# Kernel optimization log

Hardware: AMD Instinct MI355X
Metric: run time of the kernel (lower is better)

## Reference

```python
import jax, jax.numpy as jnp
import numpy as np

D_MODEL = 2048
NUM_HEADS = 16
HEAD_DIM = D_MODEL // NUM_HEADS
SEQ = 2048
BATCH = 2
ROPE_BASE = 10000.0
EPS = 1e-5


def _rope_cache(seq_len, head_dim, base):
    inv_freq = 1.0 / (base ** (jnp.arange(0, head_dim, 2, dtype=jnp.float32) / head_dim))
    t = jnp.arange(seq_len, dtype=jnp.float32)
    freqs = jnp.outer(t, inv_freq)                      # [S, hd/2]
    emb = jnp.concatenate([freqs, freqs], axis=-1)      # [S, hd]
    return jnp.cos(emb), jnp.sin(emb)


def _rotate_half(x):
    x1, x2 = jnp.split(x, 2, axis=-1)
    return jnp.concatenate([-x2, x1], axis=-1)


def setup_inputs() -> dict:
    key = jax.random.key(0)
    ks = jax.random.split(key, 8)
    s = 1.0 / np.sqrt(D_MODEL)
    inp = {
        "x": jax.random.normal(ks[0], (SEQ, BATCH, D_MODEL), dtype=jnp.float32),
        "causal_mask": jnp.triu(jnp.ones((SEQ, SEQ), dtype=jnp.bool_), k=1),
        "key_padding_mask": jnp.zeros((BATCH, SEQ), dtype=jnp.bool_),
        "norm_w": jnp.ones((D_MODEL,), dtype=jnp.float32),
        "q_w": jax.random.normal(ks[1], (D_MODEL, D_MODEL), dtype=jnp.float32) * s,
        "q_b": jnp.zeros((D_MODEL,), dtype=jnp.float32),
        "k_w": jax.random.normal(ks[2], (D_MODEL, D_MODEL), dtype=jnp.float32) * s,
        "k_b": jnp.zeros((D_MODEL,), dtype=jnp.float32),
        "v_w": jax.random.normal(ks[3], (D_MODEL, D_MODEL), dtype=jnp.float32) * s,
        "v_b": jnp.zeros((D_MODEL,), dtype=jnp.float32),
        "o_w": jax.random.normal(ks[4], (D_MODEL, D_MODEL), dtype=jnp.float32) * s,
        "o_b": jnp.zeros((D_MODEL,), dtype=jnp.float32),
    }
    return inp


def reference(x, causal_mask, key_padding_mask, norm_w, q_w, q_b, k_w, k_b, v_w, v_b, o_w, o_b):
    seq_len, batch, _ = x.shape
    # RMSNorm variant: x / (||x||_2 + eps) * w  (note: L2 norm, not RMS)
    nrm = jnp.linalg.norm(x, axis=-1, keepdims=True)
    xn = x / (nrm + EPS) * norm_w

    q = (xn @ q_w.T + q_b).reshape(seq_len, batch, NUM_HEADS, HEAD_DIM)
    k = (xn @ k_w.T + k_b).reshape(seq_len, batch, NUM_HEADS, HEAD_DIM)
    v = (xn @ v_w.T + v_b).reshape(seq_len, batch, NUM_HEADS, HEAD_DIM)

    cos, sin = _rope_cache(seq_len, HEAD_DIM, ROPE_BASE)
    cos = cos[:, None, None, :]
    sin = sin[:, None, None, :]
    q = q * cos + _rotate_half(q) * sin
    k = k * cos + _rotate_half(k) * sin

    # [S,B,H,D] -> [B,H,S,D]
    q = q.transpose(1, 2, 0, 3)
    k = k.transpose(1, 2, 0, 3)
    v = v.transpose(1, 2, 0, 3)

    scores = jnp.einsum('bhqd,bhkd->bhqk', q, k) / jnp.sqrt(jnp.float32(HEAD_DIM))
    neg_inf = jnp.float32(-jnp.inf)
    scores = jnp.where(causal_mask[None, None, :, :], neg_inf, scores)
    scores = jnp.where(key_padding_mask[:, None, None, :], neg_inf, scores)

    attn = jax.nn.softmax(scores, axis=-1)
    out = jnp.einsum('bhqk,bhkd->bhqd', attn, v)
    out = out.transpose(2, 0, 1, 3).reshape(seq_len, batch, D_MODEL)  # [S,B,D]
    return out @ o_w.T + o_b
```

## Files before the change

### kernel.cpp

```cpp
#include <hip/hip_runtime.h>
#include <hip/hip_bf16.h>
#include <cstdint>

typedef __attribute__((ext_vector_type(8))) short short8_t;
typedef __attribute__((ext_vector_type(4))) short s16x4;
typedef __attribute__((ext_vector_type(4))) float f32x4;

#define SEQ 2048
#define BATCH 2
#define DM 2048
#define NH 16
#define HD 128
#define SCALE 0.08838834764831845f

__device__ __forceinline__ short f2bf(float f) {
    union { __hip_bfloat16 h; short s; } u; u.h = __float2bfloat16(f); return u.s;
}
__device__ __forceinline__ float bf2f(short s) {
    union { short s; __hip_bfloat16 h; } u; u.s = s; return __bfloat162float(u.h);
}

__global__ void __launch_bounds__(256) prep_kernel(const float* __restrict__ qw,
                                                   const float* __restrict__ kw,
                                                   const float* __restrict__ vw,
                                                   const float* __restrict__ ow,
                                                   short* __restrict__ wqkv,
                                                   const float* __restrict__ x,
                                                   const float* __restrict__ nw,
                                                   short* __restrict__ xn,
                                                   float* __restrict__ cosT,
                                                   float* __restrict__ sinT) {
    const int bid = blockIdx.x;
    const int t = threadIdx.x;
    if (bid < 2048) {
        const int per = DM * DM / 4;
        int i = bid * 256 + t;
        const int stride = 2048 * 256;
        for (; i < 4 * per; i += stride) {
            int region = i / per;
            int off = i - region * per;
            const float* src = region == 0 ? qw : (region == 1 ? kw : (region == 2 ? vw : ow));
            float4 v = ((const float4*)src)[off];
            s16x4 o;
            o[0] = f2bf(v.x); o[1] = f2bf(v.y); o[2] = f2bf(v.z); o[3] = f2bf(v.w);
            ((s16x4*)(wqkv + (size_t)region * DM * DM))[off] = o;
        }
    } else if (bid < 2560) {
        int j = (bid - 2048) * 256 + t;
        int tpos = j >> 6, i = j & 63;
        float inv = exp2f(-(2.0f * (float)i / 128.0f) * log2f(10000.0f));
        float a = (float)tpos * inv;
        cosT[tpos * 64 + i] = cosf(a);
        sinT[tpos * 64 + i] = sinf(a);
    } else {
        __shared__ float red[4];
        int row = bid - 2560;
        const float* xr = x + (size_t)row * DM;
        short* outr = xn + (size_t)row * DM;
        float vals[8];
        float ss = 0.f;
#pragma unroll
        for (int i = 0; i < 8; ++i) { float v = xr[t + 256 * i]; vals[i] = v; ss += v * v; }
#pragma unroll
        for (int off = 1; off < 64; off <<= 1) ss += __shfl_xor(ss, off);
        int lane = t & 63, wv = t >> 6;
        if (lane == 0) red[wv] = ss;
        __syncthreads();
        float tot = red[0] + red[1] + red[2] + red[3];
        float inv = 1.f / (sqrtf(tot) + 1e-5f);
#pragma unroll
        for (int i = 0; i < 8; ++i)
            outr[t + 256 * i] = f2bf(vals[i] * inv * nw[t + 256 * i]);
    }
}

#define DSREAD(d, a) asm volatile("ds_read_b128 %0, %1" : "=v"(d) : "v"(a))

template <int MODE>
__global__ void __launch_bounds__(256) gemm_db(const short* __restrict__ A,
                                               const short* __restrict__ B,
                                               int N, int K,
                                               short* __restrict__ oq, short* __restrict__ ok,
                                               short* __restrict__ ov,
                                               const float* __restrict__ bq,
                                               const float* __restrict__ bk,
                                               const float* __restrict__ bv,
                                               float* __restrict__ outF,
                                               const float* __restrict__ bias) {
    extern __shared__ short lds[];
    const int tid = threadIdx.x;
    const int lane = tid & 63;
    const int w = tid >> 6;
    const int wr = w >> 1, wc = w & 1;
    const int brow = blockIdx.y * 128;
    const int bcol = blockIdx.x * 128;

    const short* gA[4]; const short* gB[4]; int ldsC[4];
#pragma unroll
    for (int p = 0; p < 4; ++p) {
        int c = p * 256 + tid;
        int row = c >> 3;
        int slot = (c & 7) ^ (row & 7);
        gA[p] = A + (size_t)(brow + row) * K + slot * 8;
        gB[p] = B + (size_t)(bcol + row) * K + slot * 8;
        ldsC[p] = c * 8;
    }
    const uint32_t ldsBase = (uint32_t)(uintptr_t)&lds[0];

    f32x4 acc[4][4];
#pragma unroll
    for (int i = 0; i < 4; ++i)
#pragma unroll
        for (int j = 0; j < 4; ++j) acc[i][j] = (f32x4){0.f, 0.f, 0.f, 0.f};

    const int fr = lane & 15;
    const int fs = lane >> 4;
    uint32_t aOff[4][2], bOff[4][2];
#pragma unroll
    for (int i = 0; i < 4; ++i)
#pragma unroll
        for (int ks = 0; ks < 2; ++ks) {
            int ch = (ks * 4 + fs) ^ (fr & 7);
            int ar = wr * 64 + i * 16 + fr;
            int br = wc * 64 + i * 16 + fr;
            aOff[i][ks] = ldsBase + (uint32_t)(ar * 128 + ch * 16);
            bOff[i][ks] = ldsBase + 32768u + (uint32_t)(br * 128 + ch * 16);
        }

    const int nt = K >> 6;
#pragma unroll
    for (int p = 0; p < 4; ++p)
        __builtin_amdgcn_global_load_lds((const __attribute__((address_space(1))) void*)gA[p],
                                         (__attribute__((address_space(3))) void*)(lds + ldsC[p]), 16, 0, 0);
#pragma unroll
    for (int p = 0; p < 4; ++p)
        __builtin_amdgcn_global_load_lds((const __attribute__((address_space(1))) void*)gB[p],
                                         (__attribute__((address_space(3))) void*)(lds + 16384 + ldsC[p]), 16, 0, 0);

    for (int t = 0; t < nt; ++t) {
        const int cur = t & 1;
        if (t + 1 < nt) {
            const int nb = (t + 1) & 1;
            const int kb = (t + 1) << 6;
#pragma unroll
            for (int p = 0; p < 4; ++p)
                __builtin_amdgcn_global_load_lds((const __attribute__((address_space(1))) void*)(gA[p] + kb),
                                                 (__attribute__((address_space(3))) void*)(lds + nb * 8192 + ldsC[p]), 16, 0, 0);
#pragma unroll
            for (int p = 0; p < 4; ++p)
                __builtin_amdgcn_global_load_lds((const __attribute__((address_space(1))) void*)(gB[p] + kb),
                                                 (__attribute__((address_space(3))) void*)(lds + 16384 + nb * 8192 + ldsC[p]), 16, 0, 0);
            asm volatile("s_waitcnt vmcnt(8)" ::: "memory");
        } else {
            asm volatile("s_waitcnt vmcnt(0)" ::: "memory");
        }
        __builtin_amdgcn_s_barrier();

        const uint32_t ab = (uint32_t)(cur * 16384);
        short8_t af[4][2], bfv[4][2];
#pragma unroll
        for (int i = 0; i < 4; ++i)
#pragma unroll
            for (int ks = 0; ks < 2; ++ks) DSREAD(af[i][ks], aOff[i][ks] + ab);
#pragma unroll
        for (int j = 0; j < 4; ++j)
#pragma unroll
            for (int ks = 0; ks < 2; ++ks) DSREAD(bfv[j][ks], bOff[j][ks] + ab);
        asm volatile("s_waitcnt lgkmcnt(0)" ::: "memory");
        __builtin_amdgcn_sched_barrier(0);

        __builtin_amdgcn_s_setprio(1);
#pragma unroll
        for (int ks = 0; ks < 2; ++ks)
#pragma unroll
            for (int i = 0; i < 4; ++i)
#pragma unroll
                for (int j = 0; j < 4; ++j)
                    acc[i][j] = __builtin_amdgcn_mfma_f32_16x16x32_bf16(af[i][ks], bfv[j][ks], acc[i][j], 0, 0, 0);
        __builtin_amdgcn_s_setprio(0);
        __builtin_amdgcn_s_barrier();
    }

    const int fq = (lane >> 4) * 4;
#pragma unroll
    for (int i = 0; i < 4; ++i) {
        int mrow = brow + wr * 64 + i * 16 + fq;
#pragma unroll
        for (int j = 0; j < 4; ++j) {
            int ncol = bcol + wc * 64 + j * 16 + fr;
            if (MODE == 0) {
                int which = ncol >> 11;
                int hl = ncol & 2047;
                int h = hl >> 7, d = hl & 127;
                const float* bp = which == 0 ? bq : (which == 1 ? bk : bv);
                short* dst = which == 0 ? oq : (which == 1 ? ok : ov);
                float bval = bp[hl];
#pragma unroll
                for (int jj = 0; jj < 4; ++jj) {
                    int m = mrow + jj;
                    int s = m >> 1, b = m & 1;
                    float v = acc[i][j][jj] + bval;
                    size_t idx;
                    if (which == 2)
                        idx = (((size_t)(b * NH + h)) * HD + d) * SEQ + s;
                    else
                        idx = (((size_t)(b * NH + h)) * SEQ + s) * HD + d;
                    dst[idx] = f2bf(v);
                }
            } else {
                float bval = bias[ncol];
#pragma unroll
                for (int jj = 0; jj < 4; ++jj) {
                    int m = mrow + jj;
                    outF[(size_t)m * N + ncol] = acc[i][j][jj] + bval;
                }
            }
        }
    }
}

__global__ void __launch_bounds__(256) rope_k_kernel(short* __restrict__ k,
                                                     const float* __restrict__ cosT,
                                                     const float* __restrict__ sinT) {
    int w = threadIdx.x >> 6, lane = threadIdx.x & 63;
    int idx = blockIdx.x * 4 + w;
    int s = idx & (SEQ - 1);
    size_t base = (size_t)idx * HD;
    float c = cosT[s * 64 + lane], sn = sinT[s * 64 + lane];
    float k1 = bf2f(k[base + lane]), k2 = bf2f(k[base + lane + 64]);
    k[base + lane] = f2bf(k1 * c - k2 * sn);
    k[base + lane + 64] = f2bf(k2 * c + k1 * sn);
}

__global__ void __launch_bounds__(512) attn_kernel(const short* __restrict__ Q,
                                                   const short* __restrict__ K,
                                                   const short* __restrict__ V,
                                                   const float* __restrict__ cosT,
                                                   const float* __restrict__ sinT,
                                                   short* __restrict__ AO) {
    __shared__ short Kl[64 * 136];
    __shared__ short Vt[128 * 88];
    __shared__ short Pl[8][16 * 88];

    const int bh = blockIdx.x;
    const int qt = blockIdx.y;
    const int b = bh >> 4;
    const int h = bh & 15;
    const size_t base = (size_t)bh * (SEQ * HD);
    const int tid = threadIdx.x;
    const int lane = tid & 63;
    const int w = tid >> 6;
    const int fr = lane & 15;
    const int fk = (lane >> 4) * 8;
    const int fq = (lane >> 4) * 4;
    const int qbase = qt * 128 + w * 16;
    const int qg = qbase + fr;

    const int kr = tid >> 4;
    const int kc8 = (tid & 15) * 8;
    const int vd = tid >> 3;
    const int vc8 = (tid & 7) * 8;

    short8_t qf[4];
#pragma unroll
    for (int kc = 0; kc < 4; ++kc)
        qf[kc] = *(const short8_t*)&Q[base + (size_t)(qg) * HD + kc * 32 + fk];

    {
        const float* cb = cosT + (size_t)qg * 64;
        const float* sb = sinT + (size_t)qg * 64;
#pragma unroll
        for (int kc = 0; kc < 2; ++kc) {
            float4 c0 = *(const float4*)&cb[kc * 32 + fk];
            float4 c1 = *(const float4*)&cb[kc * 32 + fk + 4];
            float4 s0 = *(const float4*)&sb[kc * 32 + fk];
            float4 s1 = *(const float4*)&sb[kc * 32 + fk + 4];
            float cv[8] = {c0.x, c0.y, c0.z, c0.w, c1.x, c1.y, c1.z, c1.w};
            float sv[8] = {s0.x, s0.y, s0.z, s0.w, s1.x, s1.y, s1.z, s1.w};
#pragma unroll
            for (int e = 0; e < 8; ++e) {
                float q1 = bf2f(qf[kc][e]), q2 = bf2f(qf[kc + 2][e]);
                qf[kc][e]     = f2bf((q1 * cv[e] - q2 * sv[e]) * SCALE);
                qf[kc + 2][e] = f2bf((q2 * cv[e] + q1 * sv[e]) * SCALE);
            }
        }
    }

    f32x4 acc[8];
#pragma unroll
    for (int dt = 0; dt < 8; ++dt) acc[dt] = (f32x4){0.f, 0.f, 0.f, 0.f};
    float m_r = -1e30f, l_r = 0.f;

    const int ktmax = qt * 2 + 1;

    short8_t kreg[2], vreg[2];
#pragma unroll
    for (int p = 0; p < 2; ++p) {
        kreg[p] = *(const short8_t*)&K[base + (size_t)(p * 32 + kr) * HD + kc8];
        vreg[p] = *(const short8_t*)&V[base + (size_t)(p * 64 + vd) * SEQ + vc8];
    }
#pragma unroll
    for (int p = 0; p < 2; ++p) {
        *(short8_t*)&Kl[(p * 32 + kr) * 136 + kc8] = kreg[p];
        *(short8_t*)&Vt[(p * 64 + vd) * 88 + vc8] = vreg[p];
    }
    __syncthreads();

    for (int kt = 0; kt <= ktmax; ++kt) {
        const bool active = (kt * 64 <= qbase + 15);
        f32x4 st[4];
        if (active) {
            __builtin_amdgcn_s_setprio(1);
#pragma unroll
            for (int nt = 0; nt < 4; ++nt) {
                f32x4 a = (f32x4){0.f, 0.f, 0.f, 0.f};
#pragma unroll
                for (int kc = 0; kc < 4; ++kc) {
                    short8_t kf = *(const short8_t*)&Kl[(nt * 16 + fr) * 136 + kc * 32 + fk];
                    a = __builtin_amdgcn_mfma_f32_16x16x32_bf16(kf, qf[kc], a, 0, 0, 0);
                }
                st[nt] = a;
            }
            __builtin_amdgcn_s_setprio(0);
        }

        if (kt < ktmax) {
            const size_t kb2 = base + (size_t)((kt + 1) * 64) * HD;
            const size_t vb2 = base + (size_t)(kt + 1) * 64;
#pragma unroll
            for (int p = 0; p < 2; ++p) {
                kreg[p] = *(const short8_t*)&K[kb2 + (size_t)(p * 32 + kr) * HD + kc8];
                vreg[p] = *(const short8_t*)&V[vb2 + (size_t)(p * 64 + vd) * SEQ + vc8];
            }
        }

        if (active) {
            const bool needMask = (kt * 64 + 63 > qbase);
            float rmax = -1e30f;
            if (needMask) {
#pragma unroll
                for (int nt = 0; nt < 4; ++nt)
#pragma unroll
                    for (int jj = 0; jj < 4; ++jj) {
                        int kg = kt * 64 + nt * 16 + fq + jj;
                        float sv = st[nt][jj];
                        sv = (kg > qg) ? -1e30f : sv;
                        st[nt][jj] = sv;
                        rmax = fmaxf(rmax, sv);
                    }
            } else {
#pragma unroll
                for (int nt = 0; nt < 4; ++nt)
#pragma unroll
                    for (int jj = 0; jj < 4; ++jj) rmax = fmaxf(rmax, st[nt][jj]);
            }
            rmax = fmaxf(rmax, __shfl_xor(rmax, 16));
            rmax = fmaxf(rmax, __shfl_xor(rmax, 32));

            const bool doRescale = !(m_r > -1e29f && __all(rmax - m_r <= 8.0f));
            float m_new = doRescale ? fmaxf(m_r, rmax) : m_r;
            float rsum = 0.f;
#pragma unroll
            for (int nt = 0; nt < 4; ++nt) {
                s16x4 pk;
#pragma unroll
                for (int jj = 0; jj < 4; ++jj) {
                    float p = __expf(st[nt][jj] - m_new);
                    rsum += p;
                    pk[jj] = f2bf(p);
                }
                *(s16x4*)&Pl[w][fr * 88 + nt * 16 + fq] = pk;
            }
            rsum += __shfl_xor(rsum, 16);
            rsum += __shfl_xor(rsum, 32);
            if (doRescale) {
                float corr = __expf(m_r - m_new);
                l_r = l_r * corr + rsum;
                m_r = m_new;
                float c4[4];
#pragma unroll
                for (int jj = 0; jj < 4; ++jj) c4[jj] = __shfl(corr, fq + jj);
#pragma unroll
                for (int dt = 0; dt < 8; ++dt)
#pragma unroll
                    for (int jj = 0; jj < 4; ++jj) acc[dt][jj] *= c4[jj];
            } else {
                l_r += rsum;
            }

            __builtin_amdgcn_s_setprio(1);
#pragma unroll
            for (int kc = 0; kc < 2; ++kc) {
                short8_t pf = *(const short8_t*)&Pl[w][fr * 88 + kc * 32 + fk];
#pragma unroll
                for (int dt = 0; dt < 8; ++dt) {
                    short8_t vf = *(const short8_t*)&Vt[(dt * 16 + fr) * 88 + kc * 32 + fk];
                    acc[dt] = __builtin_amdgcn_mfma_f32_16x16x32_bf16(pf, vf, acc[dt], 0, 0, 0);
                }
            }
            __builtin_amdgcn_s_setprio(0);
        }

        __syncthreads();
        if (kt < ktmax) {
#pragma unroll
            for (int p = 0; p < 2; ++p) {
                *(short8_t*)&Kl[(p * 32 + kr) * 136 + kc8] = kreg[p];
                *(short8_t*)&Vt[(p * 64 + vd) * 88 + vc8] = vreg[p];
            }
            __syncthreads();
        }
    }

    float linv[4];
#pragma unroll
    for (int jj = 0; jj < 4; ++jj) linv[jj] = 1.f / __shfl(l_r, fq + jj);
#pragma unroll
    for (int dt = 0; dt < 8; ++dt) {
#pragma unroll
        for (int jj = 0; jj < 4; ++jj) {
            int qrow = qbase + fq + jj;
            int d = dt * 16 + fr;
            AO[((size_t)(qrow * BATCH + b)) * DM + h * HD + d] = f2bf(acc[dt][jj] * linv[jj]);
        }
    }
}

extern "C" void kernel_launch(void* const* d_in, const int* in_sizes, int n_in,
                              void* d_out, int out_size, void* d_ws, size_t ws_size,
                              hipStream_t stream) {
    (void)in_sizes; (void)n_in; (void)out_size; (void)ws_size;
    const float* x  = (const float*)d_in[0];
    const float* nw = (const float*)d_in[3];
    const float* qw = (const float*)d_in[4];
    const float* qbias = (const float*)d_in[5];
    const float* kw = (const float*)d_in[6];
    const float* kbias = (const float*)d_in[7];
    const float* vw = (const float*)d_in[8];
    const float* vbias = (const float*)d_in[9];
    const float* ow = (const float*)d_in[10];
    const float* obias = (const float*)d_in[11];
    float* out = (float*)d_out;

    char* ws = (char*)d_ws;
    size_t off = 0;
    float* cosT = (float*)(ws + off); off += (size_t)SEQ * 64 * 4;
    float* sinT = (float*)(ws + off); off += (size_t)SEQ * 64 * 4;
    short* wqkv = (short*)(ws + off); off += (size_t)3 * DM * DM * 2;
    short* wo   = (short*)(ws + off); off += (size_t)DM * DM * 2;
    short* xn   = (short*)(ws + off); off += (size_t)SEQ * BATCH * DM * 2;
    short* qd   = (short*)(ws + off); off += (size_t)SEQ * BATCH * DM * 2;
    short* kd   = (short*)(ws + off); off += (size_t)SEQ * BATCH * DM * 2;
    short* vd   = (short*)(ws + off); off += (size_t)SEQ * BATCH * DM * 2;
    short* ao   = xn;

    hipFuncSetAttribute((const void*)gemm_db<0>, hipFuncAttributeMaxDynamicSharedMemorySize, 65536);
    hipFuncSetAttribute((const void*)gemm_db<1>, hipFuncAttributeMaxDynamicSharedMemorySize, 65536);

    prep_kernel<<<2560 + SEQ * BATCH, 256, 0, stream>>>(qw, kw, vw, ow, wqkv, x, nw, xn, cosT, sinT);
    gemm_db<0><<<dim3(3 * DM / 128, SEQ * BATCH / 128), 256, 65536, stream>>>(
        xn, wqkv, 3 * DM, DM, qd, kd, vd, qbias, kbias, vbias, nullptr, nullptr);
    rope_k_kernel<<<BATCH * NH * SEQ / 4, 256, 0, stream>>>(kd, cosT, sinT);
    attn_kernel<<<dim3(BATCH * NH, SEQ / 128), 512, 0, stream>>>(qd, kd, vd, cosT, sinT, ao);
    gemm_db<1><<<dim3(DM / 128, SEQ * BATCH / 128), 256, 65536, stream>>>(
        ao, wo, DM, DM, nullptr, nullptr, nullptr, nullptr, nullptr, nullptr, out, obias);
}
```

Measured before the change: 259.7 us.

## Replace QKV projection GEMM with 256x256-tile 8-wave ping-pong kernel

The fused QKV projection moves from the 128x128 double-buffered GEMM to a new 512-thread kernel with 256x256 output tiles and 128KB of LDS. Tiles are staged in half-blocks via direct global-to-LDS loads, interleaved with MFMA quarter-steps, and a blockIdx swizzle groups neighbouring tiles for L2 reuse. The intent is more data reuse per loaded byte and better overlap of loads with MFMA work. The cost is heavy register pressure (a 32-entry accumulator array) and delicate hand-counted waitcnt/barrier sequencing. The DSREAD constraint also becomes early-clobber.

```diff
diff --git a/kernel.cpp b/kernel.cpp
--- a/kernel.cpp
+++ b/kernel.cpp
@@ -19,6 +19,8 @@
 __device__ __forceinline__ float bf2f(short s) {
     union { short s; __hip_bfloat16 h; } u; u.s = s; return __bfloat162float(u.h);
 }
+
+#define DSREAD(d, a) asm volatile("ds_read_b128 %0, %1" : "=&v"(d) : "v"(a))
 
 __global__ void __launch_bounds__(256) prep_kernel(const float* __restrict__ qw,
                                                    const float* __restrict__ kw,
@@ -74,17 +76,224 @@
     }
 }
 
-#define DSREAD(d, a) asm volatile("ds_read_b128 %0, %1" : "=v"(d) : "v"(a))
+__device__ __forceinline__ void stage_half(const short* __restrict__ G, int gRow0, int K, int kOff,
+                                           short* ldsBase, int w, int lane) {
+#pragma unroll
+    for (int j = 0; j < 2; ++j) {
+        int c = j * 512 + w * 64 + lane;
+        int row = c >> 3;
+        int slot = (c & 7) ^ (row & 7);
+        const short* g = G + (size_t)(gRow0 + row) * K + kOff + slot * 8;
+        __builtin_amdgcn_global_load_lds((const __attribute__((address_space(1))) void*)g,
+                                         (__attribute__((address_space(3))) void*)(ldsBase + (j * 512 + w * 64) * 8),
+                                         16, 0, 0);
+    }
+}
+
+__device__ __forceinline__ void q16(f32x4 (&acc)[8][4], short8_t (&aa)[4][2], short8_t (&bb)[4][2],
+                                    int ib, int jb) {
+#pragma unroll
+    for (int ks = 0; ks < 2; ++ks)
+#pragma unroll
+        for (int ii = 0; ii < 4; ++ii)
+#pragma unroll
+            for (int jj = 0; jj < 2; ++jj)
+                acc[ib + ii][jb + jj] = __builtin_amdgcn_mfma_f32_16x16x32_bf16(
+                    aa[ii][ks], bb[jb + jj][ks], acc[ib + ii][jb + jj], 0, 0, 0);
+}
+
+template <bool LAST>
+__device__ __forceinline__ void kpair(short* lds, uint32_t uA, uint32_t uAx, uint32_t uB, uint32_t uBx,
+                                      const short* __restrict__ A, const short* __restrict__ B,
+                                      int brow, int bcol, int K, int it,
+                                      f32x4 (&acc)[8][4], int w, int lane) {
+    const int t1 = 2 * it + 1, p0 = 2 * it + 2, p1 = 2 * it + 3;
+    short* ldsA = lds;
+    short* ldsB = lds + 32768;
+    short8_t af[4][2], bf[4][2], ag[4][2];
+
+#pragma unroll
+    for (int i = 0; i < 4; ++i) { DSREAD(af[i][0], uA + i * 2048); DSREAD(af[i][1], uAx + i * 2048); }
+#pragma unroll
+    for (int j = 0; j < 2; ++j) { DSREAD(bf[j][0], uB + j * 2048); DSREAD(bf[j][1], uBx + j * 2048); }
+    stage_half(A, brow + 128, K, t1 * 64, ldsA + 24576, w, lane);
+    asm volatile("s_waitcnt lgkmcnt(8)" ::: "memory");
+    __builtin_amdgcn_s_barrier();
+    asm volatile("s_waitcnt lgkmcnt(0)" ::: "memory");
+    __builtin_amdgcn_sched_barrier(0);
+    __builtin_amdgcn_s_setprio(1);
+    q16(acc, af, bf, 0, 0);
+    __builtin_amdgcn_s_setprio(0);
+    __builtin_amdgcn_s_barrier();
+
+#pragma unroll
+    for (int j = 2; j < 4; ++j) { DSREAD(bf[j][0], uB + j * 2048); DSREAD(bf[j][1], uBx + j * 2048); }
+    __builtin_amdgcn_s_barrier();
+    asm volatile("s_waitcnt lgkmcnt(0)" ::: "memory");
+    __builtin_amdgcn_sched_barrier(0);
+    __builtin_amdgcn_s_setprio(1);
+    q16(acc, af, bf, 0, 2);
+    __builtin_amdgcn_s_setprio(0);
+    __builtin_amdgcn_s_barrier();
+
+#pragma unroll
+    for (int i = 0; i < 4; ++i) { DSREAD(ag[i][0], uA + (i + 4) * 2048); DSREAD(ag[i][1], uAx + (i + 4) * 2048); }
+    if (!LAST) stage_half(B, bcol, K, p0 * 64, ldsB, w, lane);
+    __builtin_amdgcn_s_barrier();
+    asm volatile("s_waitcnt lgkmcnt(0)" ::: "memory");
+    __builtin_amdgcn_sched_barrier(0);
+    __builtin_amdgcn_s_setprio(1);
+    q16(acc, ag, bf, 4, 0);
+    __builtin_amdgcn_s_setprio(0);
+    __builtin_amdgcn_s_barrier();
+
+    if (!LAST) {
+        stage_half(B, bcol + 128, K, p0 * 64, ldsB + 8192, w, lane);
+        stage_half(A, brow, K, p0 * 64, ldsA, w, lane);
+    }
+    __builtin_amdgcn_s_barrier();
+    __builtin_amdgcn_s_setprio(1);
+    q16(acc, ag, bf, 4, 2);
+    __builtin_amdgcn_s_setprio(0);
+    if (!LAST) asm volatile("s_waitcnt vmcnt(6)" ::: "memory");
+    else       asm volatile("s_waitcnt vmcnt(0)" ::: "memory");
+    __builtin_amdgcn_s_barrier();
+
+#pragma unroll
+    for (int i = 0; i < 4; ++i) { DSREAD(af[i][0], uA + 32768 + i * 2048); DSREAD(af[i][1], uAx + 32768 + i * 2048); }
+#pragma unroll
+    for (int j = 0; j < 2; ++j) { DSREAD(bf[j][0], uB + 32768 + j * 2048); DSREAD(bf[j][1], uBx + 32768 + j * 2048); }
+    if (!LAST) stage_half(A, brow + 128, K, p0 * 64, ldsA + 8192, w, lane);
+    asm volatile("s_waitcnt lgkmcnt(8)" ::: "memory");
+    __builtin_amdgcn_s_barrier();
+    asm volatile("s_waitcnt lgkmcnt(0)" ::: "memory");
+    __builtin_amdgcn_sched_barrier(0);
+    __builtin_amdgcn_s_setprio(1);
+    q16(acc, af, bf, 0, 0);
+    __builtin_amdgcn_s_setprio(0);
+    __builtin_amdgcn_s_barrier();
+
+#pragma unroll
+    for (int j = 2; j < 4; ++j) { DSREAD(bf[j][0], uB + 32768 + j * 2048); DSREAD(bf[j][1], uBx + 32768 + j * 2048); }
+    __builtin_amdgcn_s_barrier();
+    asm volatile("s_waitcnt lgkmcnt(0)" ::: "memory");
+    __builtin_amdgcn_sched_barrier(0);
+    __builtin_amdgcn_s_setprio(1);
+    q16(acc, af, bf, 0, 2);
+    __builtin_amdgcn_s_setprio(0);
+    __builtin_amdgcn_s_barrier();
+
+#pragma unroll
+    for (int i = 0; i < 4; ++i) { DSREAD(ag[i][0], uA + 32768 + (i + 4) * 2048); DSREAD(ag[i][1], uAx + 32768 + (i + 4) * 2048); }
+    if (!LAST) stage_half(B, bcol, K, p1 * 64, ldsB + 16384, w, lane);
+    __builtin_amdgcn_s_barrier();
+    asm volatile("s_waitcnt lgkmcnt(0)" ::: "memory");
+    __builtin_amdgcn_sched_barrier(0);
+    __builtin_amdgcn_s_setprio(1);
+    q16(acc, ag, bf, 4, 0);
+    __builtin_amdgcn_s_setprio(0);
+    __builtin_amdgcn_s_barrier();
+
+    if (!LAST) {
+        stage_half(B, bcol + 128, K, p1 * 64, ldsB + 24576, w, lane);
+        stage_half(A, brow, K, p1 * 64, ldsA + 16384, w, lane);
+    }
+    __builtin_amdgcn_s_barrier();
+    __builtin_amdgcn_s_setprio(1);
+    q16(acc, ag, bf, 4, 2);
+    __builtin_amdgcn_s_setprio(0);
+    if (!LAST) asm volatile("s_waitcnt vmcnt(6)" ::: "memory");
+    __builtin_amdgcn_s_barrier();
+}
+
+__global__ void __launch_bounds__(512, 2) gemm8p(const short* __restrict__ A,
+                                                 const short* __restrict__ B,
+                                                 int Mt, int Nt, int K,
+                                                 short* __restrict__ oq, short* __restrict__ ok,
+                                                 short* __restrict__ ov,
+                                                 const float* __restrict__ bq,
+                                                 const float* __restrict__ bk,
+                                                 const float* __restrict__ bv) {
+    extern __shared__ short lds[];
+    const int tid = threadIdx.x;
+    const int lane = tid & 63;
+    const int w = tid >> 6;
+    const int wr = w >> 2;
+    const int wc = w & 3;
+
+    const int nwg = Mt * Nt;
+    const int cpx = nwg >> 3;
+    const int bid = blockIdx.x;
+    const int swz = (bid & 7) * cpx + (bid >> 3);
+    const int brow = (swz % Mt) * 256;
+    const int bcol = (swz / Mt) * 256;
+
+    f32x4 acc[8][4];
+#pragma unroll
+    for (int i = 0; i < 8; ++i)
+#pragma unroll
+        for (int j = 0; j < 4; ++j) acc[i][j] = (f32x4){0.f, 0.f, 0.f, 0.f};
+
+    short* ldsA = lds;
+    short* ldsB = lds + 32768;
+
+    const int fr = lane & 15;
+    const int fs = lane >> 4;
+    const int c0 = fs ^ (fr & 7);
+    const uint32_t ldsBase = (uint32_t)(uintptr_t)&lds[0];
+    const uint32_t uA  = ldsBase + (uint32_t)(wr * 16384 + fr * 128 + c0 * 16);
+    const uint32_t uAx = ldsBase + (uint32_t)(wr * 16384 + fr * 128 + (c0 ^ 4) * 16);
+    const uint32_t uB  = ldsBase + 65536u + (uint32_t)((wc >> 1) * 16384 + (wc & 1) * 8192 + fr * 128 + c0 * 16);
+    const uint32_t uBx = ldsBase + 65536u + (uint32_t)((wc >> 1) * 16384 + (wc & 1) * 8192 + fr * 128 + (c0 ^ 4) * 16);
+
+    stage_half(B, bcol,       K, 0,  ldsB,          w, lane);
+    stage_half(B, bcol + 128, K, 0,  ldsB + 8192,   w, lane);
+    stage_half(A, brow,       K, 0,  ldsA,          w, lane);
+    stage_half(A, brow + 128, K, 0,  ldsA + 8192,   w, lane);
+    stage_half(B, bcol,       K, 64, ldsB + 16384,  w, lane);
+    stage_half(B, bcol + 128, K, 64, ldsB + 24576,  w, lane);
+    stage_half(A, brow,       K, 64, ldsA + 16384,  w, lane);
+    asm volatile("s_waitcnt vmcnt(6)" ::: "memory");
+    __builtin_amdgcn_s_barrier();
+
+    const int niter = K / 128;
+    for (int it = 0; it < niter - 1; ++it)
+        kpair<false>(lds, uA, uAx, uB, uBx, A, B, brow, bcol, K, it, acc, w, lane);
+    kpair<true>(lds, uA, uAx, uB, uBx, A, B, brow, bcol, K, niter - 1, acc, w, lane);
+
+    const int fq = (lane >> 4) * 4;
+#pragma unroll
+    for (int i = 0; i < 8; ++i) {
+        int mrow = brow + wr * 128 + i * 16 + fq;
+#pragma unroll
+        for (int j = 0; j < 4; ++j) {
+            int ncol = bcol + wc * 64 + j * 16 + fr;
+            int which = ncol >> 11;
+            int hl = ncol & 2047;
+            int h = hl >> 7, d = hl & 127;
+            const float* bp = which == 0 ? bq : (which == 1 ? bk : bv);
+            short* dst = which == 0 ? oq : (which == 1 ? ok : ov);
+            float bval = bp[hl];
+#pragma unroll
+            for (int jj = 0; jj < 4; ++jj) {
+                int m = mrow + jj;
+                int s = m >> 1, b = m & 1;
+                float v = acc[i][j][jj] + bval;
+                size_t idx;
+                if (which == 2)
+                    idx = (((size_t)(b * NH + h)) * HD + d) * SEQ + s;
+                else
+                    idx = (((size_t)(b * NH + h)) * SEQ + s) * HD + d;
+                dst[idx] = f2bf(v);
+            }
+        }
+    }
+}
 
 template <int MODE>
 __global__ void __launch_bounds__(256) gemm_db(const short* __restrict__ A,
                                                const short* __restrict__ B,
                                                int N, int K,
-                                               short* __restrict__ oq, short* __restrict__ ok,
-                                               short* __restrict__ ov,
-                                               const float* __restrict__ bq,
-                                               const float* __restrict__ bk,
-                                               const float* __restrict__ bv,
                                                float* __restrict__ outF,
                                                const float* __restrict__ bias) {
     extern __shared__ short lds[];
@@ -188,32 +397,11 @@
 #pragma unroll
         for (int j = 0; j < 4; ++j) {
             int ncol = bcol + wc * 64 + j * 16 + fr;
-            if (MODE == 0) {
-                int which = ncol >> 11;
-                int hl = ncol & 2047;
-                int h = hl >> 7, d = hl & 127;
-                const float* bp = which == 0 ? bq : (which == 1 ? bk : bv);
-                short* dst = which == 0 ? oq : (which == 1 ? ok : ov);
-                float bval = bp[hl];
-#pragma unroll
-                for (int jj = 0; jj < 4; ++jj) {
-                    int m = mrow + jj;
-                    int s = m >> 1, b = m & 1;
-                    float v = acc[i][j][jj] + bval;
-                    size_t idx;
-                    if (which == 2)
-                        idx = (((size_t)(b * NH + h)) * HD + d) * SEQ + s;
-                    else
-                        idx = (((size_t)(b * NH + h)) * SEQ + s) * HD + d;
-                    dst[idx] = f2bf(v);
-                }
-            } else {
-                float bval = bias[ncol];
-#pragma unroll
-                for (int jj = 0; jj < 4; ++jj) {
-                    int m = mrow + jj;
-                    outF[(size_t)m * N + ncol] = acc[i][j][jj] + bval;
-                }
+            float bval = bias[ncol];
+#pragma unroll
+            for (int jj = 0; jj < 4; ++jj) {
+                int m = mrow + jj;
+                outF[(size_t)m * N + ncol] = acc[i][j][jj] + bval;
             }
         }
     }
@@ -454,14 +642,14 @@
     short* vd   = (short*)(ws + off); off += (size_t)SEQ * BATCH * DM * 2;
     short* ao   = xn;
 
-    hipFuncSetAttribute((const void*)gemm_db<0>, hipFuncAttributeMaxDynamicSharedMemorySize, 65536);
+    hipFuncSetAttribute((const void*)gemm8p, hipFuncAttributeMaxDynamicSharedMemorySize, 131072);
     hipFuncSetAttribute((const void*)gemm_db<1>, hipFuncAttributeMaxDynamicSharedMemorySize, 65536);
 
     prep_kernel<<<2560 + SEQ * BATCH, 256, 0, stream>>>(qw, kw, vw, ow, wqkv, x, nw, xn, cosT, sinT);
-    gemm_db<0><<<dim3(3 * DM / 128, SEQ * BATCH / 128), 256, 65536, stream>>>(
-        xn, wqkv, 3 * DM, DM, qd, kd, vd, qbias, kbias, vbias, nullptr, nullptr);
+    gemm8p<<<dim3(16 * 24), 512, 131072, stream>>>(
+        xn, wqkv, 16, 24, DM, qd, kd, vd, qbias, kbias, vbias);
     rope_k_kernel<<<BATCH * NH * SEQ / 4, 256, 0, stream>>>(kd, cosT, sinT);
     attn_kernel<<<dim3(BATCH * NH, SEQ / 128), 512, 0, stream>>>(qd, kd, vd, cosT, sinT, ao);
     gemm_db<1><<<dim3(DM / 128, SEQ * BATCH / 128), 256, 65536, stream>>>(
-        ao, wo, DM, DM, nullptr, nullptr, nullptr, nullptr, nullptr, nullptr, out, obias);
-}
+        ao, wo, DM, DM, out, obias);
+}
```

New measurement: 424.0 us. +63.3%, slower.
